# Kernel tuning notes

Measured on AMD Instinct MI355X. Metric: run time of the kernel, lower is better.

## Reference

```python
import jax, jax.numpy as jnp
import numpy as np

HEADS1, HID = 2, 128
OUT_FEATS = 256
K, M = 8, 128


def _gat_conv(x, src, dst, W, a_src, a_dst, bias, heads, out_dim, concat, neg_slope):
    """PyG-style GATConv: linear -> per-edge leakyrelu attention -> dst-softmax -> scatter-sum."""
    N = x.shape[0]
    h = (x @ W.T).reshape(N, heads, out_dim)          # [N, H, D]
    alpha_src = jnp.sum(h * a_src, axis=-1)            # [N, H]
    alpha_dst = jnp.sum(h * a_dst, axis=-1)            # [N, H]
    e = jax.nn.leaky_relu(alpha_src[src] + alpha_dst[dst], neg_slope)  # [E, H]
    # numerically stable segment softmax over incoming edges per destination
    m = jax.ops.segment_max(e, dst, num_segments=N)    # [N, H]
    e = jnp.exp(e - m[dst])
    s = jax.ops.segment_sum(e, dst, num_segments=N)    # [N, H]
    alpha = e / s[dst]                                  # [E, H]
    msg = h[src] * alpha[:, :, None]                    # [E, H, D]
    out = jax.ops.segment_sum(msg, dst, num_segments=N)  # [N, H, D]
    out = out.reshape(N, heads * out_dim) if concat else out.mean(axis=1)
    return out + bias


def setup_inputs() -> dict:
    key = jax.random.key(0)
    ks = jax.random.split(key, 14)
    N, E, IN = 50000, 800000, 256
    x = jax.random.normal(ks[0], (N, IN), dtype=jnp.float32)
    edge_index = jax.random.randint(ks[1], (2, E), 0, N, dtype=jnp.int64)
    sc = 0.1
    return {
        "x": x,
        "edge_index": edge_index,
        "W1": jax.random.normal(ks[2], (HEADS1 * HID, IN), dtype=jnp.float32) * sc,
        "a_src1": jax.random.normal(ks[3], (HEADS1, HID), dtype=jnp.float32) * sc,
        "a_dst1": jax.random.normal(ks[4], (HEADS1, HID), dtype=jnp.float32) * sc,
        "b1": jax.random.normal(ks[5], (HEADS1 * HID,), dtype=jnp.float32) * sc,
        "W2": jax.random.normal(ks[6], (OUT_FEATS, HEADS1 * HID), dtype=jnp.float32) * sc,
        "a_src2": jax.random.normal(ks[7], (1, OUT_FEATS), dtype=jnp.float32) * sc,
        "a_dst2": jax.random.normal(ks[8], (1, OUT_FEATS), dtype=jnp.float32) * sc,
        "b2": jax.random.normal(ks[9], (OUT_FEATS,), dtype=jnp.float32) * sc,
        "g": jax.random.normal(ks[10], (OUT_FEATS, K * M), dtype=jnp.float32) * sc,
        "mu": jax.random.normal(ks[11], (K, M), dtype=jnp.float32) * sc,
    }


def reference(x, edge_index, W1, a_src1, a_dst1, b1, W2, a_src2, a_dst2, b2, g, mu):
    N = x.shape[0]
    loops = jnp.arange(N, dtype=edge_index.dtype)  # PyG GATConv adds self-loops by default
    src = jnp.concatenate([edge_index[0], loops])
    dst = jnp.concatenate([edge_index[1], loops])
    h = _gat_conv(x, src, dst, W1, a_src1, a_dst1, b1, HEADS1, HID, True, 0.2)
    h = jax.nn.leaky_relu(h, 0.01)  # F.leaky_relu default slope
    h = _gat_conv(h, src, dst, W2, a_src2, a_dst2, b2, 1, OUT_FEATS, False, 0.2)
    out = (h @ g).reshape(N, K, M)                      # [N, K, M]
    # cosine similarity against mu along M (torch eps=1e-8)
    num = jnp.einsum('nkm,km->nk', out, mu)
    denom = jnp.maximum(
        jnp.linalg.norm(out, axis=-1) * jnp.linalg.norm(mu, axis=-1)[None, :], 1e-8
    )
    return num / denom  # [N, K]
```

## Files before the change

### kernel.cpp

```cpp
#include <hip/hip_runtime.h>
#include <math.h>

typedef short s16x8 __attribute__((ext_vector_type(8)));
typedef float f32x4 __attribute__((ext_vector_type(4)));

__device__ __forceinline__ float lrelu(float x, float s) { return x > 0.0f ? x : s * x; }

__device__ __forceinline__ unsigned short f2bf(float f) {
  unsigned int u = __float_as_uint(f);
  u = (u + 0x7FFFu + ((u >> 16) & 1u)) >> 16;
  return (unsigned short)u;
}
__device__ __forceinline__ float bf2f(unsigned short h) {
  return __uint_as_float(((unsigned int)h) << 16);
}

__device__ __forceinline__ void gload_lds16(void* lds, const void* g) {
  __builtin_amdgcn_global_load_lds(
      (const __attribute__((address_space(1))) unsigned int*)g,
      (__attribute__((address_space(3))) unsigned int*)lds, 16, 0, 0);
}

__global__ void deg_kernel(const int* __restrict__ dst, int* __restrict__ deg, int E) {
  int e = blockIdx.x * blockDim.x + threadIdx.x;
  if (e < E) atomicAdd(&deg[dst[e]], 1);
}

__global__ __launch_bounds__(1024) void scan_kernel(const int* __restrict__ deg,
                                                    int* __restrict__ rowptr, int N) {
  __shared__ int sums[1024];
  int t = threadIdx.x;
  int CH = (N + 1023) / 1024;
  int base = t * CH;
  int s = 0;
  for (int i = 0; i < CH; ++i) { int idx = base + i; if (idx < N) s += deg[idx]; }
  sums[t] = s;
  __syncthreads();
  for (int off = 1; off < 1024; off <<= 1) {
    int v = (t >= off) ? sums[t - off] : 0;
    __syncthreads();
    sums[t] += v;
    __syncthreads();
  }
  int run = (t == 0) ? 0 : sums[t - 1];
  for (int i = 0; i < CH; ++i) {
    int idx = base + i;
    if (idx < N) { rowptr[idx] = run; run += deg[idx]; }
  }
  if (t == 1023) rowptr[N] = sums[1023];
}

__global__ void fill_kernel(const int* __restrict__ src, const int* __restrict__ dst,
                            int* __restrict__ cursor, int* __restrict__ colsrc, int E) {
  int e = blockIdx.x * blockDim.x + threadIdx.x;
  if (e < E) {
    int d = dst[e];
    int pos = atomicAdd(&cursor[d], 1);
    colsrc[pos] = src[e];
  }
}

__global__ void cvt_rows_kernel(const float* __restrict__ src, unsigned short* __restrict__ dst,
                                int nrows, int prows) {
  int t = blockIdx.x * blockDim.x + threadIdx.x;
  int row = t >> 6;
  int c = (t & 63) * 4;
  if (row >= prows) return;
  float4 v = make_float4(0.f, 0.f, 0.f, 0.f);
  if (row < nrows) v = *(const float4*)&src[(size_t)row * 256 + c];
  ushort4 o;
  o.x = f2bf(v.x); o.y = f2bf(v.y); o.z = f2bf(v.z); o.w = f2bf(v.w);
  *(ushort4*)&dst[(size_t)row * 256 + c] = o;
}

__global__ void cvt_gT_kernel(const float* __restrict__ g, unsigned short* __restrict__ gT) {
  int idx = blockIdx.x * blockDim.x + threadIdx.x;
  int k = idx >> 10, n = idx & 1023;
  gT[(size_t)n * 256 + k] = f2bf(g[idx]);
}

template<int EPI, int AH>
__global__ __launch_bounds__(256, 2) void gemm_bf16(
    const unsigned short* __restrict__ A, const unsigned short* __restrict__ B,
    unsigned short* __restrict__ Cb,
    const float* __restrict__ avs, const float* __restrict__ avd,
    float* __restrict__ asrcO, float* __restrict__ adstO,
    const float* __restrict__ mu, const float* __restrict__ nmu,
    float* __restrict__ outcos, int M)
{
  __shared__ unsigned short As[128 * 64];
  __shared__ unsigned short Bs[128 * 64];
  const int t = threadIdx.x;
  const int w = t >> 6;
  const int l = t & 63;
  const int m0 = blockIdx.x * 128;
  const int n0 = blockIdx.y * 128;

  f32x4 acc[2][8];
  #pragma unroll
  for (int i = 0; i < 2; ++i)
    #pragma unroll
    for (int j = 0; j < 8; ++j) acc[i][j] = (f32x4){0.f, 0.f, 0.f, 0.f};

  const unsigned char* Ab = (const unsigned char*)A;
  const unsigned char* Bb = (const unsigned char*)B;
  unsigned char* AsB = (unsigned char*)As;
  unsigned char* BsB = (unsigned char*)Bs;

  const int srow = l >> 3;
  const int gchk = (l & 7) ^ srow;

  for (int kb = 0; kb < 256; kb += 64) {
    #pragma unroll
    for (int i = 0; i < 4; ++i) {
      int seg = w * 4 + i;
      int row = seg * 8 + srow;
      gload_lds16(AsB + seg * 1024,
                  Ab + (size_t)(m0 + row) * 512 + kb * 2 + gchk * 16);
      gload_lds16(BsB + seg * 1024,
                  Bb + (size_t)(n0 + row) * 512 + kb * 2 + gchk * 16);
    }
    asm volatile("s_waitcnt vmcnt(0)" ::: "memory");
    __syncthreads();

    const int rl = l & 15;
    const int kc = l >> 4;
    #pragma unroll
    for (int ks = 0; ks < 2; ++ks) {
      s16x8 af[2], bfr[8];
      #pragma unroll
      for (int mf = 0; mf < 2; ++mf) {
        int r = w * 32 + mf * 16 + rl;
        int slot = (ks * 4 + kc) ^ (r & 7);
        af[mf] = *(const s16x8*)&As[r * 64 + slot * 8];
      }
      #pragma unroll
      for (int nf = 0; nf < 8; ++nf) {
        int r = nf * 16 + rl;
        int slot = (ks * 4 + kc) ^ (r & 7);
        bfr[nf] = *(const s16x8*)&Bs[r * 64 + slot * 8];
      }
      #pragma unroll
      for (int mf = 0; mf < 2; ++mf)
        #pragma unroll
        for (int nf = 0; nf < 8; ++nf)
          acc[mf][nf] = __builtin_amdgcn_mfma_f32_16x16x32_bf16(af[mf], bfr[nf], acc[mf][nf], 0, 0, 0);
    }
    __syncthreads();
  }

  if (EPI == 0) {
    #pragma unroll
    for (int mf = 0; mf < 2; ++mf)
      #pragma unroll
      for (int nf = 0; nf < 8; ++nf)
        #pragma unroll
        for (int j = 0; j < 4; ++j) {
          int r = m0 + w * 32 + mf * 16 + (l >> 4) * 4 + j;
          int c = n0 + nf * 16 + (l & 15);
          Cb[(size_t)r * 256 + c] = f2bf(acc[mf][nf][j]);
        }
    if (AH > 0) {
      float avS[8], avD[8];
      #pragma unroll
      for (int nf = 0; nf < 8; ++nf) {
        avS[nf] = avs[n0 + nf * 16 + (l & 15)];
        avD[nf] = avd[n0 + nf * 16 + (l & 15)];
      }
      #pragma unroll
      for (int mf = 0; mf < 2; ++mf)
        #pragma unroll
        for (int j = 0; j < 4; ++j) {
          float ds = 0.f, dd = 0.f;
          #pragma unroll
          for (int nf = 0; nf < 8; ++nf) {
            float o = acc[mf][nf][j];
            ds = fmaf(o, avS[nf], ds);
            dd = fmaf(o, avD[nf], dd);
          }
          #pragma unroll
          for (int off = 1; off < 16; off <<= 1) {
            ds += __shfl_xor(ds, off, 64);
            dd += __shfl_xor(dd, off, 64);
          }
          if ((l & 15) == 0) {
            int r = m0 + w * 32 + mf * 16 + (l >> 4) * 4 + j;
            if (r < M) {
              if (AH == 2) {
                asrcO[(size_t)r * 2 + blockIdx.y] = ds;
                adstO[(size_t)r * 2 + blockIdx.y] = dd;
              } else {
                atomicAdd(&asrcO[r], ds);
                atomicAdd(&adstO[r], dd);
              }
            }
          }
        }
    }
  } else {
    const int kchunk = blockIdx.y;
    float nm = nmu[kchunk];
    float mv[8];
    #pragma unroll
    for (int nf = 0; nf < 8; ++nf) mv[nf] = mu[kchunk * 128 + nf * 16 + (l & 15)];
    #pragma unroll
    for (int mf = 0; mf < 2; ++mf)
      #pragma unroll
      for (int j = 0; j < 4; ++j) {
        float num = 0.f, ss = 0.f;
        #pragma unroll
        for (int nf = 0; nf < 8; ++nf) {
          float o = acc[mf][nf][j];
          num = fmaf(o, mv[nf], num);
          ss  = fmaf(o, o, ss);
        }
        #pragma unroll
        for (int off = 1; off < 16; off <<= 1) {
          num += __shfl_xor(num, off, 64);
          ss  += __shfl_xor(ss, off, 64);
        }
        if ((l & 15) == 0) {
          int r = m0 + w * 32 + mf * 16 + (l >> 4) * 4 + j;
          if (r < M) outcos[(size_t)r * 8 + kchunk] = num / fmaxf(sqrtf(ss) * nm, 1e-8f);
        }
      }
  }
}

template<int H, bool OUT_LRELU>
__global__ __launch_bounds__(256) void agg_kernel(
    const unsigned short* __restrict__ hin, const float* __restrict__ asrc,
    const float* __restrict__ adst, const int* __restrict__ rowptr,
    const int* __restrict__ colsrc, const float* __restrict__ bias,
    unsigned short* __restrict__ outp, int N)
{
  int wid  = threadIdx.x >> 6;
  int lane = threadIdx.x & 63;
  int n = blockIdx.x * 4 + wid;
  if (n >= N) return;
  const int half = lane >> 5;
  const int fl   = lane & 31;
  const int head = (H == 2) ? (fl >> 4) : 0;

  int beg = rowptr[n], end = rowptr[n + 1];

  float ad0 = adst[(size_t)n * H + 0];
  float ad1 = (H == 2) ? adst[(size_t)n * 2 + 1] : 0.f;
  float m0 = lrelu(asrc[(size_t)n * H + 0] + ad0, 0.2f);
  float m1 = (H == 2) ? lrelu(asrc[(size_t)n * 2 + 1] + ad1, 0.2f) : 0.f;
  float s0 = 1.f, s1 = 1.f;

  float acc[8];
  {
    s16x8 hv = *(const s16x8*)&hin[(size_t)n * 256 + fl * 8];
    #pragma unroll
    for (int k = 0; k < 8; ++k)
      acc[k] = (half == 0) ? bf2f((unsigned short)hv[k]) : 0.f;
  }

  for (int cbeg = beg; cbeg < end; cbeg += 64) {
    int cnt = end - cbeg; if (cnt > 64) cnt = 64;
    int src_i = 0;
    float e0 = -1e30f, e1 = -1e30f;
    if (lane < cnt) {
      src_i = colsrc[cbeg + lane];
      if (H == 2) {
        float2 av = *(const float2*)&asrc[(size_t)src_i * 2];
        e0 = lrelu(av.x + ad0, 0.2f);
        e1 = lrelu(av.y + ad1, 0.2f);
      } else {
        e0 = lrelu(asrc[src_i] + ad0, 0.2f);
      }
    }
    float c0 = e0, c1 = e1;
    #pragma unroll
    for (int off = 32; off >= 1; off >>= 1) {
      c0 = fmaxf(c0, __shfl_xor(c0, off, 64));
      if (H == 2) c1 = fmaxf(c1, __shfl_xor(c1, off, 64));
    }
    float nm0 = fmaxf(m0, c0);
    float r0 = __expf(m0 - nm0); m0 = nm0;
    float r1 = 1.f;
    if (H == 2) { float nm1 = fmaxf(m1, c1); r1 = __expf(m1 - nm1); m1 = nm1; }
    s0 *= r0; if (H == 2) s1 *= r1;
    float rh = (H == 2 && head) ? r1 : r0;
    #pragma unroll
    for (int k = 0; k < 8; ++k) acc[k] *= rh;
    float p0 = (lane < cnt) ? __expf(e0 - m0) : 0.f;
    float p1 = (H == 2 && lane < cnt) ? __expf(e1 - m1) : 0.f;
    float t0 = p0, t1 = p1;
    #pragma unroll
    for (int off = 32; off >= 1; off >>= 1) {
      t0 += __shfl_xor(t0, off, 64);
      if (H == 2) t1 += __shfl_xor(t1, off, 64);
    }
    s0 += t0; if (H == 2) s1 += t1;

    int npair = (cnt + 1) >> 1;
    int pi = 0;
    for (; pi + 2 <= npair; pi += 2) {
      int ia = pi * 2, ib = pi * 2 + 2;
      int sa0 = __shfl(src_i, ia, 64),     sa1 = __shfl(src_i, ia + 1, 64);
      int sb0 = __shfl(src_i, ib, 64),     sb1 = __shfl(src_i, ib + 1, 64);
      float qa00 = __shfl(p0, ia, 64),     qa01 = __shfl(p0, ia + 1, 64);
      float qb00 = __shfl(p0, ib, 64),     qb01 = __shfl(p0, ib + 1, 64);
      float wA, wB;
      if (H == 2) {
        float qa10 = __shfl(p1, ia, 64), qa11 = __shfl(p1, ia + 1, 64);
        float qb10 = __shfl(p1, ib, 64), qb11 = __shfl(p1, ib + 1, 64);
        wA = head ? (half ? qa11 : qa10) : (half ? qa01 : qa00);
        wB = head ? (half ? qb11 : qb10) : (half ? qb01 : qb00);
      } else {
        wA = half ? qa01 : qa00;
        wB = half ? qb01 : qb00;
      }
      int sjA = half ? sa1 : sa0;
      int sjB = half ? sb1 : sb0;
      s16x8 vA = *(const s16x8*)&hin[(size_t)sjA * 256 + fl * 8];
      s16x8 vB = *(const s16x8*)&hin[(size_t)sjB * 256 + fl * 8];
      #pragma unroll
      for (int k = 0; k < 8; ++k) acc[k] = fmaf(bf2f((unsigned short)vA[k]), wA, acc[k]);
      #pragma unroll
      for (int k = 0; k < 8; ++k) acc[k] = fmaf(bf2f((unsigned short)vB[k]), wB, acc[k]);
    }
    for (; pi < npair; ++pi) {
      int ia = pi * 2;
      int sa0 = __shfl(src_i, ia, 64), sa1 = __shfl(src_i, ia + 1, 64);
      float qa00 = __shfl(p0, ia, 64), qa01 = __shfl(p0, ia + 1, 64);
      float wA;
      if (H == 2) {
        float qa10 = __shfl(p1, ia, 64), qa11 = __shfl(p1, ia + 1, 64);
        wA = head ? (half ? qa11 : qa10) : (half ? qa01 : qa00);
      } else {
        wA = half ? qa01 : qa00;
      }
      int sjA = half ? sa1 : sa0;
      s16x8 vA = *(const s16x8*)&hin[(size_t)sjA * 256 + fl * 8];
      #pragma unroll
      for (int k = 0; k < 8; ++k) acc[k] = fmaf(bf2f((unsigned short)vA[k]), wA, acc[k]);
    }
  }

  float sh = (H == 2 && head) ? s1 : s0;
  float inv = 1.0f / sh;
  #pragma unroll
  for (int k = 0; k < 8; ++k) acc[k] += __shfl_xor(acc[k], 32, 64);
  if (half == 0) {
    float bv[8];
    *(float4*)&bv[0] = *(const float4*)&bias[fl * 8];
    *(float4*)&bv[4] = *(const float4*)&bias[fl * 8 + 4];
    s16x8 o;
    #pragma unroll
    for (int k = 0; k < 8; ++k) {
      float v = acc[k] * inv + bv[k];
      if (OUT_LRELU) v = lrelu(v, 0.01f);
      o[k] = (short)f2bf(v);
    }
    *(s16x8*)&outp[(size_t)n * 256 + fl * 8] = o;
  }
}

__global__ __launch_bounds__(64) void munorm_kernel(const float* __restrict__ mu,
                                                    float* __restrict__ norm_mu) {
  int lane = threadIdx.x;
  for (int k = 0; k < 8; ++k) {
    float v0 = mu[k * 128 + lane];
    float v1 = mu[k * 128 + 64 + lane];
    float s = v0 * v0 + v1 * v1;
    #pragma unroll
    for (int off = 1; off < 64; off <<= 1) s += __shfl_xor(s, off, 64);
    if (lane == 0) norm_mu[k] = sqrtf(s);
  }
}

extern "C" void kernel_launch(void* const* d_in, const int* in_sizes, int n_in,
                              void* d_out, int out_size, void* d_ws, size_t ws_size,
                              hipStream_t stream) {
  const float* x      = (const float*)d_in[0];
  const int*   ei     = (const int*)  d_in[1];
  const float* W1     = (const float*)d_in[2];
  const float* a_src1 = (const float*)d_in[3];
  const float* a_dst1 = (const float*)d_in[4];
  const float* b1     = (const float*)d_in[5];
  const float* W2     = (const float*)d_in[6];
  const float* a_src2 = (const float*)d_in[7];
  const float* a_dst2 = (const float*)d_in[8];
  const float* b2     = (const float*)d_in[9];
  const float* g      = (const float*)d_in[10];
  const float* mu     = (const float*)d_in[11];

  const int N  = in_sizes[0] / 256;
  const int E  = in_sizes[1] / 2;
  const int Mp = ((N + 127) / 128) * 128;
  const int* src = ei;
  const int* dst = ei + E;

  unsigned short* us = (unsigned short*)d_ws;
  size_t off = 0;
  unsigned short* xb  = us + off; off += (size_t)Mp * 256;
  unsigned short* h1b = us + off; off += (size_t)Mp * 256;
  unsigned short* o1b = us + off; off += (size_t)Mp * 256;
  unsigned short* h2b = us + off; off += (size_t)Mp * 256;
  unsigned short* o2b = xb;
  float* f = (float*)(us + off);
  size_t fo = 0;
  float* asrc1 = f + fo; fo += (size_t)N * 2;
  float* adst1 = f + fo; fo += (size_t)N * 2;
  float* asrc2 = f + fo; fo += N;
  float* adst2 = f + fo; fo += N;
  float* nmu   = f + fo; fo += 8;
  int* deg    = (int*)(f + fo);
  int* rowptr = deg + N;
  int* cursor = rowptr + N + 1;
  int* colsrc = cursor + N;
  unsigned short* w1b = (unsigned short*)(colsrc + E);
  unsigned short* w2b = w1b + 256 * 256;
  unsigned short* gTb = w2b + 256 * 256;

  hipMemsetAsync(deg, 0, (size_t)N * sizeof(int), stream);
  hipMemsetAsync(asrc2, 0, (size_t)N * 2 * sizeof(float), stream);
  deg_kernel<<<(E + 255) / 256, 256, 0, stream>>>(dst, deg, E);
  scan_kernel<<<1, 1024, 0, stream>>>(deg, rowptr, N);
  hipMemcpyAsync(cursor, rowptr, (size_t)N * sizeof(int), hipMemcpyDeviceToDevice, stream);
  fill_kernel<<<(E + 255) / 256, 256, 0, stream>>>(src, dst, cursor, colsrc, E);

  cvt_rows_kernel<<<Mp / 4, 256, 0, stream>>>(x, xb, N, Mp);
  cvt_rows_kernel<<<64, 256, 0, stream>>>(W1, w1b, 256, 256);
  cvt_rows_kernel<<<64, 256, 0, stream>>>(W2, w2b, 256, 256);
  cvt_gT_kernel<<<1024, 256, 0, stream>>>(g, gTb);
  munorm_kernel<<<1, 64, 0, stream>>>(mu, nmu);

  const int gm = Mp / 128;

  gemm_bf16<0, 2><<<dim3(gm, 2), 256, 0, stream>>>(xb, w1b, h1b,
      a_src1, a_dst1, asrc1, adst1, nullptr, nullptr, nullptr, N);
  agg_kernel<2, true><<<(N + 3) / 4, 256, 0, stream>>>(h1b, asrc1, adst1, rowptr, colsrc, b1, o1b, N);

  gemm_bf16<0, 1><<<dim3(gm, 2), 256, 0, stream>>>(o1b, w2b, h2b,
      a_src2, a_dst2, asrc2, adst2, nullptr, nullptr, nullptr, N);
  agg_kernel<1, false><<<(N + 3) / 4, 256, 0, stream>>>(h2b, asrc2, adst2, rowptr, colsrc, b2, o2b, N);

  gemm_bf16<1, 0><<<dim3(gm, 8), 256, 0, stream>>>(o2b, gTb, nullptr,
      nullptr, nullptr, nullptr, nullptr, mu, nmu, (float*)d_out, N);
}
```

Baseline: 502.3 us.

## Replace single-block degree scan with three-phase multi-block scan

The single 1024-thread block scan, in which each thread walked a strided chunk of about 49 degrees serially, is replaced by a block-sum kernel, a single-block scan of the block sums, and a per-block scan that writes the final offsets. The last kernel writes rowptr and cursor together, so the device-to-device copy of rowptr into cursor goes away. This spreads the scan across many CUs at the cost of two extra kernel launches. The scan of block sums assumes at most 256 blocks, which holds for N=50000 (196 blocks).

```diff
diff --git a/kernel.cpp b/kernel.cpp
--- a/kernel.cpp
+++ b/kernel.cpp
@@ -26,28 +26,56 @@
   if (e < E) atomicAdd(&deg[dst[e]], 1);
 }
 
-__global__ __launch_bounds__(1024) void scan_kernel(const int* __restrict__ deg,
-                                                    int* __restrict__ rowptr, int N) {
-  __shared__ int sums[1024];
+__global__ __launch_bounds__(256) void bsum_kernel(const int* __restrict__ deg,
+                                                   int* __restrict__ bsum, int N) {
+  int t = blockIdx.x * 256 + threadIdx.x;
+  int v = (t < N) ? deg[t] : 0;
+  #pragma unroll
+  for (int off = 1; off < 64; off <<= 1) v += __shfl_xor(v, off, 64);
+  __shared__ int ws[4];
+  if ((threadIdx.x & 63) == 0) ws[threadIdx.x >> 6] = v;
+  __syncthreads();
+  if (threadIdx.x == 0) bsum[blockIdx.x] = ws[0] + ws[1] + ws[2] + ws[3];
+}
+
+__global__ __launch_bounds__(256) void bscan_kernel(const int* __restrict__ bsum,
+                                                    int* __restrict__ boff, int nb,
+                                                    int* __restrict__ rowptr_total) {
+  __shared__ int s[256];
   int t = threadIdx.x;
-  int CH = (N + 1023) / 1024;
-  int base = t * CH;
-  int s = 0;
-  for (int i = 0; i < CH; ++i) { int idx = base + i; if (idx < N) s += deg[idx]; }
-  sums[t] = s;
+  int v = (t < nb) ? bsum[t] : 0;
+  s[t] = v;
   __syncthreads();
-  for (int off = 1; off < 1024; off <<= 1) {
-    int v = (t >= off) ? sums[t - off] : 0;
-    __syncthreads();
-    sums[t] += v;
-    __syncthreads();
-  }
-  int run = (t == 0) ? 0 : sums[t - 1];
-  for (int i = 0; i < CH; ++i) {
-    int idx = base + i;
-    if (idx < N) { rowptr[idx] = run; run += deg[idx]; }
-  }
-  if (t == 1023) rowptr[N] = sums[1023];
+  for (int off = 1; off < 256; off <<= 1) {
+    int u = (t >= off) ? s[t - off] : 0;
+    __syncthreads();
+    s[t] += u;
+    __syncthreads();
+  }
+  if (t < nb) boff[t] = s[t] - v;
+  if (t == nb - 1) *rowptr_total = s[t];
+}
+
+__global__ __launch_bounds__(256) void bwrite_kernel(const int* __restrict__ deg,
+                                                     const int* __restrict__ boff,
+                                                     int* __restrict__ rowptr,
+                                                     int* __restrict__ cursor, int N) {
+  __shared__ int s[256];
+  int t = blockIdx.x * 256 + threadIdx.x;
+  int v = (t < N) ? deg[t] : 0;
+  s[threadIdx.x] = v;
+  __syncthreads();
+  for (int off = 1; off < 256; off <<= 1) {
+    int u = (threadIdx.x >= off) ? s[threadIdx.x - off] : 0;
+    __syncthreads();
+    s[threadIdx.x] += u;
+    __syncthreads();
+  }
+  if (t < N) {
+    int ex = boff[blockIdx.x] + s[threadIdx.x] - v;
+    rowptr[t] = ex;
+    cursor[t] = ex;
+  }
 }
 
 __global__ void fill_kernel(const int* __restrict__ src, const int* __restrict__ dst,
@@ -392,6 +420,7 @@
   const int N  = in_sizes[0] / 256;
   const int E  = in_sizes[1] / 2;
   const int Mp = ((N + 127) / 128) * 128;
+  const int nb = (N + 255) / 256;
   const int* src = ei;
   const int* dst = ei + E;
 
@@ -413,15 +442,18 @@
   int* rowptr = deg + N;
   int* cursor = rowptr + N + 1;
   int* colsrc = cursor + N;
-  unsigned short* w1b = (unsigned short*)(colsrc + E);
+  int* bsum   = colsrc + E;
+  int* boff   = bsum + 256;
+  unsigned short* w1b = (unsigned short*)(boff + 256);
   unsigned short* w2b = w1b + 256 * 256;
   unsigned short* gTb = w2b + 256 * 256;
 
   hipMemsetAsync(deg, 0, (size_t)N * sizeof(int), stream);
   hipMemsetAsync(asrc2, 0, (size_t)N * 2 * sizeof(float), stream);
   deg_kernel<<<(E + 255) / 256, 256, 0, stream>>>(dst, deg, E);
-  scan_kernel<<<1, 1024, 0, stream>>>(deg, rowptr, N);
-  hipMemcpyAsync(cursor, rowptr, (size_t)N * sizeof(int), hipMemcpyDeviceToDevice, stream);
+  bsum_kernel<<<nb, 256, 0, stream>>>(deg, bsum, N);
+  bscan_kernel<<<1, 256, 0, stream>>>(bsum, boff, nb, rowptr + N);
+  bwrite_kernel<<<nb, 256, 0, stream>>>(deg, boff, rowptr, cursor, N);
   fill_kernel<<<(E + 255) / 256, 256, 0, stream>>>(src, dst, cursor, colsrc, E);
 
   cvt_rows_kernel<<<Mp / 4, 256, 0, stream>>>(x, xb, N, Mp);
```

After: 413.7 us. 17.6% less time.
